# Kernel optimization log

Hardware: AMD Instinct MI355X
Metric: run time of the kernel (lower is better)

## Reference

```python
import jax, jax.numpy as jnp
import numpy as np

# PyTorch LSTM cell with zero initial (h, c): W_hh @ h0 == 0, and c = sigmoid(i)*tanh(g)
# since the forget-gate term f*c0 vanishes. Gate order in torch: i, f, g, o.
# b here is the combined b_ih + b_hh (identical math).

def lstm_step0(x, Wih, b):
    pre = x @ Wih.T + b                      # (N, 4H)
    i, f, g, o = jnp.split(pre, 4, axis=-1)
    c = jax.nn.sigmoid(i) * jnp.tanh(g)
    return jax.nn.sigmoid(o) * jnp.tanh(c)   # (N, H)


def setup_inputs() -> dict:
    key = jax.random.key(0)
    ks = jax.random.split(key, 13)
    num_ts, num_periods, F = 128, 256, 128
    GH, NH, NF = 512, 256, 10
    s = lambda k, shape, fan: (jax.random.normal(k, shape, jnp.float32) / np.sqrt(fan))
    return {
        "X": jax.random.normal(ks[0], (num_ts, num_periods, F), jnp.float32),
        "g_Wih0": s(ks[1], (4 * GH, F), F),
        "g_b0": s(ks[2], (4 * GH,), GH),
        "g_Wih1": s(ks[3], (4 * GH, GH), GH),
        "g_b1": s(ks[4], (4 * GH,), GH),
        "aff_W": s(ks[5], (NF, GH), GH),
        "aff_b": s(ks[6], (NF,), GH),
        "n_Wih0": s(ks[7], (4 * NH, F), F),
        "n_b0": s(ks[8], (4 * NH,), NH),
        "n_Wih1": s(ks[9], (4 * NH, NH), NH),
        "n_b1": s(ks[10], (4 * NH,), NH),
        "noise_W": s(ks[11], (1, NH), NH),
        "noise_b": s(ks[12], (1,), NH),
    }


def reference(X, g_Wih0, g_b0, g_Wih1, g_b1, aff_W, aff_b,
              n_Wih0, n_b0, n_Wih1, n_b1, noise_W, noise_b):
    num_ts, num_periods, num_feats = X.shape
    x = X.reshape(-1, num_feats)             # (num_ts*num_periods, F)

    # Global factor branch: 2-layer LSTM single step from zero state
    hg = lstm_step0(lstm_step0(x, g_Wih0, g_b0), g_Wih1, g_b1)
    hg = jax.nn.relu(hg)
    mus = (hg @ aff_W.T + aff_b).sum(axis=-1).reshape(num_ts, num_periods)

    # Noise branch: 2-layer LSTM single step from zero state
    hn = lstm_step0(lstm_step0(x, n_Wih0, n_b0), n_Wih1, n_b1)
    hn = jax.nn.relu(hn)
    sigmas = jax.nn.softplus(hn @ noise_W.T + noise_b)  # log(1+exp(.)), stable
    sigmas = sigmas.reshape(num_ts, num_periods) + 1e-6
    return mus, sigmas
```

## Files before the change

### kernel.cpp

```cpp
#include <hip/hip_runtime.h>
#include <hip/hip_bf16.h>
#include <hip/hip_fp16.h>

typedef _Float16 h8_t __attribute__((ext_vector_type(8)));
typedef _Float16 h4_t __attribute__((ext_vector_type(4)));
typedef float f4_t __attribute__((ext_vector_type(4)));

#define M_ROWS 32768

__device__ __forceinline__ void gload_lds16(const void* g, void* l) {
  __builtin_amdgcn_global_load_lds((const __attribute__((address_space(1))) void*)g,
                                   (__attribute__((address_space(3))) void*)l, 16, 0, 0);
}

__device__ __forceinline__ float sigmoid_f(float x) { return 1.f / (1.f + __expf(-x)); }
__device__ __forceinline__ float tanh_f(float x) { return 1.f - 2.f / (__expf(2.f * x) + 1.f); }

struct GArgs {
  const _Float16* A;
  const _Float16* W;
  const float* bias;
  _Float16* Hout;
  const float* rvec;
  float* partial;
};

__global__ void prep_all(const float* __restrict__ X, const float* __restrict__ gW0,
                         const float* __restrict__ gW1, const float* __restrict__ nW0,
                         const float* __restrict__ nW1, const float* __restrict__ aff_W,
                         const float* __restrict__ aff_b,
                         _Float16* __restrict__ Xh, _Float16* __restrict__ Wg0,
                         _Float16* __restrict__ Wg1, _Float16* __restrict__ Wn0,
                         _Float16* __restrict__ Wn1,
                         float* __restrict__ pg, float* __restrict__ pn,
                         float* __restrict__ wsum) {
  int b = blockIdx.x;
  const float* s; _Float16* d; int base;
  if (b < 4096)      { s = X;   d = Xh;  base = b; }
  else if (b < 4352) { s = gW0; d = Wg0; base = b - 4096; }
  else if (b < 5376) { s = gW1; d = Wg1; base = b - 4352; }
  else if (b < 5504) { s = nW0; d = Wn0; base = b - 5376; }
  else if (b < 5760) { s = nW1; d = Wn1; base = b - 5504; }
  else if (b < 5888) {
    int i = (b - 5760) * 256 + threadIdx.x;
    pg[i] = 0.f; pn[i] = 0.f;
    return;
  } else {
    int j = (b - 5888) * 256 + threadIdx.x;
    float sum = 0.f;
#pragma unroll
    for (int r = 0; r < 10; ++r) sum += aff_W[r * 512 + j];
    wsum[j] = sum;
    if (j == 0) {
      float bs = 0.f;
#pragma unroll
      for (int r = 0; r < 10; ++r) bs += aff_b[r];
      wsum[512] = bs;
    }
    return;
  }
  int i4 = (base * 256 + threadIdx.x) * 4;
  float4 v = *(const float4*)(s + i4);
  h4_t o;
  o[0] = (_Float16)v.x; o[1] = (_Float16)v.y; o[2] = (_Float16)v.z; o[3] = (_Float16)v.w;
  *(h4_t*)(d + i4) = o;
}

template <int K_DIM, int H_DIM, bool FUSE, int NMT>
__device__ __forceinline__ void gemm_body(const GArgs& ga, int h0, int m_base,
                                          _Float16* As, _Float16* Bs) {
  const int tid = threadIdx.x;
  const int wid = tid >> 6;
  const int lane = tid & 63;
  const int wave_m = wid >> 1;
  const int wave_h = wid & 1;
  const int q = lane >> 4;
  const int tcol = lane & 15;

  constexpr int NT = K_DIM / 64;
  constexpr int TOT = NMT * NT;
  constexpr bool BREUSE = (NMT > 1) && (NT == 2);
  constexpr int A_BYTES = 128 * 64 * 2;
  constexpr int B_BYTES = 3 * 64 * 64 * 2;
  constexpr int A_ELEMS = 128 * 64;
  constexpr int B_ELEMS = 3 * 64 * 64;

  const _Float16* aptr[2]; int aoff[2];
#pragma unroll
  for (int c = 0; c < 2; ++c) {
    int o = ((wid * 2 + c) << 10) + (lane << 4);
    int row = o >> 7, pch = (o >> 4) & 7;
    int lch = pch ^ (row & 7);
    aptr[c] = ga.A + (size_t)(m_base + row) * K_DIM + lch * 8;
    aoff[c] = o;
  }
  const _Float16* bptr[3]; int boff[3];
#pragma unroll
  for (int c = 0; c < 3; ++c) {
    int o = ((wid * 3 + c) << 10) + (lane << 4);
    int pan = o >> 13;
    int row = (o >> 7) & 63, pch = (o >> 4) & 7;
    int lch = pch ^ (row & 7);
    int gbase = (pan == 0 ? 0 : (pan == 1 ? 2 * H_DIM : 3 * H_DIM)) + h0 + row;
    bptr[c] = ga.W + (size_t)gbase * K_DIM + lch * 8;
    boff[c] = o;
  }
  int a_rd[2][2];
#pragma unroll
  for (int ks = 0; ks < 2; ++ks)
#pragma unroll
    for (int mi = 0; mi < 2; ++mi) {
      int r = wave_m * 32 + mi * 16 + tcol;
      int c = ks * 4 + q;
      a_rd[ks][mi] = r * 64 + (c ^ (r & 7)) * 8;
    }
  int b_rd[2][2];
#pragma unroll
  for (int ks = 0; ks < 2; ++ks)
#pragma unroll
    for (int ni = 0; ni < 2; ++ni) {
      int j = wave_h * 32 + ni * 16 + tcol;
      int c = ks * 4 + q;
      b_rd[ks][ni] = j * 64 + (c ^ (j & 7)) * 8;
    }

  const int jcol0 = h0 + wave_h * 32;
  float ebi[2], ebg[2], ebo[2], erv[2];
  if constexpr (NMT > 1) {
#pragma unroll
    for (int ni = 0; ni < 2; ++ni) {
      int j = jcol0 + ni * 16 + tcol;
      ebi[ni] = ga.bias[j];
      ebg[ni] = ga.bias[2 * H_DIM + j];
      ebo[ni] = ga.bias[3 * H_DIM + j];
      if constexpr (FUSE) erv[ni] = ga.rvec[j];
    }
  }

  f4_t acc[3][2][2];
#pragma unroll
  for (int p = 0; p < 3; ++p)
#pragma unroll
    for (int mi = 0; mi < 2; ++mi)
#pragma unroll
      for (int ni = 0; ni < 2; ++ni) acc[p][mi][ni] = (f4_t){0.f, 0.f, 0.f, 0.f};

#pragma unroll
  for (int c = 0; c < 2; ++c) gload_lds16(aptr[c], (char*)As + aoff[c]);
#pragma unroll
  for (int c = 0; c < 3; ++c) gload_lds16(bptr[c], (char*)Bs + boff[c]);
#pragma unroll
  for (int c = 0; c < 2; ++c) aptr[c] += 64;
#pragma unroll
  for (int c = 0; c < 3; ++c) bptr[c] += 64;

#pragma unroll
  for (int s = 0; s < TOT; ++s) {
    const int cur = s & 1;
    const int nxt = cur ^ 1;
    if (s < TOT - 1) {
      const bool stB = (!BREUSE) || (s + 1 < NT);
#pragma unroll
      for (int c = 0; c < 2; ++c) gload_lds16(aptr[c], (char*)As + nxt * A_BYTES + aoff[c]);
      if (stB) {
#pragma unroll
        for (int c = 0; c < 3; ++c) gload_lds16(bptr[c], (char*)Bs + nxt * B_BYTES + boff[c]);
      }
      if (((s + 2) % NT) == 0) {
#pragma unroll
        for (int c = 0; c < 2; ++c) aptr[c] += 128 * K_DIM - (NT - 1) * 64;
      } else {
#pragma unroll
        for (int c = 0; c < 2; ++c) aptr[c] += 64;
      }
      if (stB) {
        if (((s + 2) % NT) == 0) {
#pragma unroll
          for (int c = 0; c < 3; ++c) bptr[c] -= (NT - 1) * 64;
        } else {
#pragma unroll
          for (int c = 0; c < 3; ++c) bptr[c] += 64;
        }
      }
      if (stB) asm volatile("s_waitcnt vmcnt(5)" ::: "memory");
      else     asm volatile("s_waitcnt vmcnt(2)" ::: "memory");
    } else {
      asm volatile("s_waitcnt vmcnt(0)" ::: "memory");
    }
    __builtin_amdgcn_s_barrier();
    asm volatile("" ::: "memory");

#pragma unroll
    for (int ks = 0; ks < 2; ++ks) {
      h8_t af[2];
#pragma unroll
      for (int mi = 0; mi < 2; ++mi) af[mi] = *(const h8_t*)&As[cur * A_ELEMS + a_rd[ks][mi]];
#pragma unroll
      for (int p = 0; p < 3; ++p) {
#pragma unroll
        for (int ni = 0; ni < 2; ++ni) {
          h8_t bf = *(const h8_t*)&Bs[cur * B_ELEMS + p * 4096 + b_rd[ks][ni]];
#pragma unroll
          for (int mi = 0; mi < 2; ++mi)
            acc[p][mi][ni] = __builtin_amdgcn_mfma_f32_16x16x32_f16(af[mi], bf, acc[p][mi][ni], 0, 0, 0);
        }
      }
    }
    asm volatile("" ::: "memory");

    if ((s % NT) == NT - 1) {
      const int mm = s / NT;
      const int mrow0 = m_base + mm * 128 + wave_m * 32;
      if constexpr (!FUSE) {
#pragma unroll
        for (int ni = 0; ni < 2; ++ni) {
          int j = jcol0 + ni * 16 + tcol;
          float bi, bg, bo;
          if constexpr (NMT > 1) { bi = ebi[ni]; bg = ebg[ni]; bo = ebo[ni]; }
          else { bi = ga.bias[j]; bg = ga.bias[2 * H_DIM + j]; bo = ga.bias[3 * H_DIM + j]; }
#pragma unroll
          for (int mi = 0; mi < 2; ++mi)
#pragma unroll
            for (int r = 0; r < 4; ++r) {
              float pi = acc[0][mi][ni][r] + bi;
              float pgt = acc[1][mi][ni][r] + bg;
              float po = acc[2][mi][ni][r] + bo;
              float cc = sigmoid_f(pi) * tanh_f(pgt);
              float hh = sigmoid_f(po) * tanh_f(cc);
              int m = mrow0 + mi * 16 + q * 4 + r;
              ga.Hout[(size_t)m * H_DIM + j] = (_Float16)hh;
            }
        }
      } else {
        float rsum[2][4];
#pragma unroll
        for (int mi = 0; mi < 2; ++mi)
#pragma unroll
          for (int r = 0; r < 4; ++r) rsum[mi][r] = 0.f;
#pragma unroll
        for (int ni = 0; ni < 2; ++ni) {
          int j = jcol0 + ni * 16 + tcol;
          float bi, bg, bo, rv;
          if constexpr (NMT > 1) { bi = ebi[ni]; bg = ebg[ni]; bo = ebo[ni]; rv = erv[ni]; }
          else { bi = ga.bias[j]; bg = ga.bias[2 * H_DIM + j]; bo = ga.bias[3 * H_DIM + j]; rv = ga.rvec[j]; }
#pragma unroll
          for (int mi = 0; mi < 2; ++mi)
#pragma unroll
            for (int r = 0; r < 4; ++r) {
              float pi = acc[0][mi][ni][r] + bi;
              float pgt = acc[1][mi][ni][r] + bg;
              float po = acc[2][mi][ni][r] + bo;
              float cc = sigmoid_f(pi) * tanh_f(pgt);
              float hh = sigmoid_f(po) * tanh_f(cc);
              hh = fmaxf(hh, 0.f);
              rsum[mi][r] += hh * rv;
            }
        }
#pragma unroll
        for (int mi = 0; mi < 2; ++mi)
#pragma unroll
          for (int r = 0; r < 4; ++r) {
            float v = rsum[mi][r];
            v += __shfl_xor(v, 1);
            v += __shfl_xor(v, 2);
            v += __shfl_xor(v, 4);
            v += __shfl_xor(v, 8);
            if (tcol == 0) atomicAdd(&ga.partial[mrow0 + mi * 16 + q * 4 + r], v);
          }
      }
      if (s < TOT - 1) {
#pragma unroll
        for (int p = 0; p < 3; ++p)
#pragma unroll
          for (int mi = 0; mi < 2; ++mi)
#pragma unroll
            for (int ni = 0; ni < 2; ++ni) acc[p][mi][ni] = (f4_t){0.f, 0.f, 0.f, 0.f};
      }
    }

    if (s < TOT - 1) __builtin_amdgcn_s_barrier();
  }
}

__device__ __forceinline__ void swizzle_xy(int& x, int& y) {
  int lin = blockIdx.y * gridDim.x + blockIdx.x;
  int c = lin & 7;
  int r = lin >> 3;
  int xpx = gridDim.x >> 3;
  y = r % 12;
  x = c * xpx + r / 12;
}

__global__ __launch_bounds__(512, 4) void layer1_fused(GArgs g, GArgs n) {
  __shared__ __align__(16) _Float16 As[2 * 128 * 64];
  __shared__ __align__(16) _Float16 Bs[2 * 3 * 64 * 64];
  int x, y; swizzle_xy(x, y);
  if (y < 8) gemm_body<128, 512, false, 2>(g, y * 64, x * 256, As, Bs);
  else       gemm_body<128, 256, false, 2>(n, (y - 8) * 64, x * 256, As, Bs);
}

__global__ __launch_bounds__(512, 4) void layer2_fused(GArgs g, GArgs n) {
  __shared__ __align__(16) _Float16 As[2 * 128 * 64];
  __shared__ __align__(16) _Float16 Bs[2 * 3 * 64 * 64];
  int x, y; swizzle_xy(x, y);
  if (y < 8) gemm_body<512, 512, true, 1>(g, y * 64, x * 128, As, Bs);
  else       gemm_body<256, 256, true, 1>(n, (y - 8) * 64, x * 128, As, Bs);
}

__global__ void finalize(const float* __restrict__ pg, const float* __restrict__ pn,
                         const float* __restrict__ wsum, const float* __restrict__ noise_b,
                         float* __restrict__ out) {
  int i = blockIdx.x * blockDim.x + threadIdx.x;
  out[i] = pg[i] + wsum[512];
  float x = pn[i] + noise_b[0];
  float sp = fmaxf(x, 0.f) + log1pf(expf(-fabsf(x)));
  out[M_ROWS + i] = sp + 1e-6f;
}

extern "C" void kernel_launch(void* const* d_in, const int* in_sizes, int n_in,
                              void* d_out, int out_size, void* d_ws, size_t ws_size,
                              hipStream_t stream) {
  const float* X       = (const float*)d_in[0];
  const float* g_Wih0  = (const float*)d_in[1];
  const float* g_b0    = (const float*)d_in[2];
  const float* g_Wih1  = (const float*)d_in[3];
  const float* g_b1    = (const float*)d_in[4];
  const float* aff_W   = (const float*)d_in[5];
  const float* aff_b   = (const float*)d_in[6];
  const float* n_Wih0  = (const float*)d_in[7];
  const float* n_b0    = (const float*)d_in[8];
  const float* n_Wih1  = (const float*)d_in[9];
  const float* n_b1    = (const float*)d_in[10];
  const float* noise_W = (const float*)d_in[11];
  const float* noise_b = (const float*)d_in[12];
  float* out = (float*)d_out;

  char* w = (char*)d_ws;
  _Float16* Xh  = (_Float16*)w; w += (size_t)M_ROWS * 128 * 2;
  _Float16* Wg0 = (_Float16*)w; w += 2048 * 128 * 2;
  _Float16* Wg1 = (_Float16*)w; w += 2048 * 512 * 2;
  _Float16* Wn0 = (_Float16*)w; w += 1024 * 128 * 2;
  _Float16* Wn1 = (_Float16*)w; w += 1024 * 256 * 2;
  _Float16* h1g = (_Float16*)w; w += (size_t)M_ROWS * 512 * 2;
  _Float16* h1n = (_Float16*)w; w += (size_t)M_ROWS * 256 * 2;
  float* pg   = (float*)w; w += (size_t)M_ROWS * 4;
  float* pn   = (float*)w; w += (size_t)M_ROWS * 4;
  float* wsum = (float*)w; w += 4096;

  prep_all<<<5890, 256, 0, stream>>>(X, g_Wih0, g_Wih1, n_Wih0, n_Wih1, aff_W, aff_b,
                                     Xh, Wg0, Wg1, Wn0, Wn1, pg, pn, wsum);

  GArgs l1g = {Xh, Wg0, g_b0, h1g, nullptr, nullptr};
  GArgs l1n = {Xh, Wn0, n_b0, h1n, nullptr, nullptr};
  layer1_fused<<<dim3(128, 12), 512, 0, stream>>>(l1g, l1n);

  GArgs l2g = {h1g, Wg1, g_b1, nullptr, wsum, pg};
  GArgs l2n = {h1n, Wn1, n_b1, nullptr, noise_W, pn};
  layer2_fused<<<dim3(256, 12), 512, 0, stream>>>(l2g, l2n);

  finalize<<<M_ROWS / 256, 256, 0, stream>>>(pg, pn, wsum, noise_b, out);
}
```

Before: 266.0 us.

## Restructure layer-1 GEMM to keep A tile resident and sweep weight panels

Replaces the layer-1 kernel with a panel kernel that loads a 128-row block of X (full K=128) into LDS once. Each block then iterates over six 64-column weight panels that span both the global and noise branches, double-buffering only the weight tiles. The goal is to cut redundant reloads of the X rows and reduce grid launch granularity. It also removes the register-cached bias values in favour of per-epilogue loads, and generalises the block swizzle to use gridDim.y. In exchange, each block runs a longer serial loop with less block-level parallelism (512 blocks).

```diff
diff --git a/kernel.cpp b/kernel.cpp
--- a/kernel.cpp
+++ b/kernel.cpp
@@ -125,17 +125,6 @@
     }
 
   const int jcol0 = h0 + wave_h * 32;
-  float ebi[2], ebg[2], ebo[2], erv[2];
-  if constexpr (NMT > 1) {
-#pragma unroll
-    for (int ni = 0; ni < 2; ++ni) {
-      int j = jcol0 + ni * 16 + tcol;
-      ebi[ni] = ga.bias[j];
-      ebg[ni] = ga.bias[2 * H_DIM + j];
-      ebo[ni] = ga.bias[3 * H_DIM + j];
-      if constexpr (FUSE) erv[ni] = ga.rvec[j];
-    }
-  }
 
   f4_t acc[3][2][2];
 #pragma unroll
@@ -215,9 +204,9 @@
 #pragma unroll
         for (int ni = 0; ni < 2; ++ni) {
           int j = jcol0 + ni * 16 + tcol;
-          float bi, bg, bo;
-          if constexpr (NMT > 1) { bi = ebi[ni]; bg = ebg[ni]; bo = ebo[ni]; }
-          else { bi = ga.bias[j]; bg = ga.bias[2 * H_DIM + j]; bo = ga.bias[3 * H_DIM + j]; }
+          float bi = ga.bias[j];
+          float bg = ga.bias[2 * H_DIM + j];
+          float bo = ga.bias[3 * H_DIM + j];
 #pragma unroll
           for (int mi = 0; mi < 2; ++mi)
 #pragma unroll
@@ -240,9 +229,10 @@
 #pragma unroll
         for (int ni = 0; ni < 2; ++ni) {
           int j = jcol0 + ni * 16 + tcol;
-          float bi, bg, bo, rv;
-          if constexpr (NMT > 1) { bi = ebi[ni]; bg = ebg[ni]; bo = ebo[ni]; rv = erv[ni]; }
-          else { bi = ga.bias[j]; bg = ga.bias[2 * H_DIM + j]; bo = ga.bias[3 * H_DIM + j]; rv = ga.rvec[j]; }
+          float bi = ga.bias[j];
+          float bg = ga.bias[2 * H_DIM + j];
+          float bo = ga.bias[3 * H_DIM + j];
+          float rv = ga.rvec[j];
 #pragma unroll
           for (int mi = 0; mi < 2; ++mi)
 #pragma unroll
@@ -287,16 +277,163 @@
   int c = lin & 7;
   int r = lin >> 3;
   int xpx = gridDim.x >> 3;
-  y = r % 12;
-  x = c * xpx + r / 12;
-}
-
-__global__ __launch_bounds__(512, 4) void layer1_fused(GArgs g, GArgs n) {
+  y = r % gridDim.y;
+  x = c * xpx + r / gridDim.y;
+}
+
+__global__ __launch_bounds__(512, 4) void layer1_panel(GArgs g, GArgs n) {
   __shared__ __align__(16) _Float16 As[2 * 128 * 64];
   __shared__ __align__(16) _Float16 Bs[2 * 3 * 64 * 64];
-  int x, y; swizzle_xy(x, y);
-  if (y < 8) gemm_body<128, 512, false, 2>(g, y * 64, x * 256, As, Bs);
-  else       gemm_body<128, 256, false, 2>(n, (y - 8) * 64, x * 256, As, Bs);
+  int x, yh; swizzle_xy(x, yh);
+  const int tid = threadIdx.x;
+  const int wid = tid >> 6;
+  const int lane = tid & 63;
+  const int wave_m = wid >> 1;
+  const int wave_h = wid & 1;
+  const int q = lane >> 4;
+  const int tcol = lane & 15;
+  const int m0 = x * 128;
+
+  int b_pan[3], b_row[3], b_lch[3], b_off[3];
+#pragma unroll
+  for (int c = 0; c < 3; ++c) {
+    int o = ((wid * 3 + c) << 10) + (lane << 4);
+    b_pan[c] = o >> 13;
+    b_row[c] = (o >> 7) & 63;
+    int pch = (o >> 4) & 7;
+    b_lch[c] = pch ^ (b_row[c] & 7);
+    b_off[c] = o;
+  }
+  int a_rd[2][2];
+#pragma unroll
+  for (int ks = 0; ks < 2; ++ks)
+#pragma unroll
+    for (int mi = 0; mi < 2; ++mi) {
+      int r = wave_m * 32 + mi * 16 + tcol;
+      int c = ks * 4 + q;
+      a_rd[ks][mi] = r * 64 + (c ^ (r & 7)) * 8;
+    }
+  int b_rd[2][2];
+#pragma unroll
+  for (int ks = 0; ks < 2; ++ks)
+#pragma unroll
+    for (int ni = 0; ni < 2; ++ni) {
+      int j = wave_h * 32 + ni * 16 + tcol;
+      int c = ks * 4 + q;
+      b_rd[ks][ni] = j * 64 + (c ^ (j & 7)) * 8;
+    }
+
+  f4_t acc[3][2][2];
+#pragma unroll
+  for (int p = 0; p < 3; ++p)
+#pragma unroll
+    for (int mi = 0; mi < 2; ++mi)
+#pragma unroll
+      for (int ni = 0; ni < 2; ++ni) acc[p][mi][ni] = (f4_t){0.f, 0.f, 0.f, 0.f};
+
+#pragma unroll
+  for (int kt = 0; kt < 2; ++kt)
+#pragma unroll
+    for (int c = 0; c < 2; ++c) {
+      int o = ((wid * 2 + c) << 10) + (lane << 4);
+      int row = o >> 7, pch = (o >> 4) & 7;
+      int lch = pch ^ (row & 7);
+      gload_lds16(g.A + (size_t)(m0 + row) * 128 + kt * 64 + lch * 8,
+                  (char*)As + kt * 16384 + o);
+    }
+  {
+    const int pnl = yh * 6;
+    const _Float16* W = pnl < 8 ? g.W : n.W;
+    const int H = pnl < 8 ? 512 : 256;
+    const int h0 = pnl < 8 ? pnl * 64 : (pnl - 8) * 64;
+#pragma unroll
+    for (int c = 0; c < 3; ++c) {
+      int gb = b_pan[c] == 0 ? 0 : (b_pan[c] == 1 ? 2 * H : 3 * H);
+      gload_lds16(W + (size_t)(gb + h0 + b_row[c]) * 128 + b_lch[c] * 8,
+                  (char*)Bs + b_off[c]);
+    }
+  }
+
+#pragma unroll
+  for (int s = 0; s < 12; ++s) {
+    const int kt = s & 1;
+    const int cur = s & 1;
+    const int pnl = yh * 6 + (s >> 1);
+    if (s < 11) {
+      const int s1 = s + 1;
+      const int pnl1 = yh * 6 + (s1 >> 1);
+      const int kt1 = s1 & 1;
+      const int nxt = cur ^ 1;
+      const _Float16* W = pnl1 < 8 ? g.W : n.W;
+      const int H = pnl1 < 8 ? 512 : 256;
+      const int h0 = pnl1 < 8 ? pnl1 * 64 : (pnl1 - 8) * 64;
+#pragma unroll
+      for (int c = 0; c < 3; ++c) {
+        int gb = b_pan[c] == 0 ? 0 : (b_pan[c] == 1 ? 2 * H : 3 * H);
+        gload_lds16(W + (size_t)(gb + h0 + b_row[c]) * 128 + kt1 * 64 + b_lch[c] * 8,
+                    (char*)Bs + nxt * 24576 + b_off[c]);
+      }
+      asm volatile("s_waitcnt vmcnt(3)" ::: "memory");
+    } else {
+      asm volatile("s_waitcnt vmcnt(0)" ::: "memory");
+    }
+    __builtin_amdgcn_s_barrier();
+    asm volatile("" ::: "memory");
+
+#pragma unroll
+    for (int ks = 0; ks < 2; ++ks) {
+      h8_t af[2];
+#pragma unroll
+      for (int mi = 0; mi < 2; ++mi) af[mi] = *(const h8_t*)&As[kt * 8192 + a_rd[ks][mi]];
+#pragma unroll
+      for (int p = 0; p < 3; ++p) {
+#pragma unroll
+        for (int ni = 0; ni < 2; ++ni) {
+          h8_t bf = *(const h8_t*)&Bs[cur * 12288 + p * 4096 + b_rd[ks][ni]];
+#pragma unroll
+          for (int mi = 0; mi < 2; ++mi)
+            acc[p][mi][ni] = __builtin_amdgcn_mfma_f32_16x16x32_f16(af[mi], bf, acc[p][mi][ni], 0, 0, 0);
+        }
+      }
+    }
+    asm volatile("" ::: "memory");
+
+    if (kt == 1) {
+      const GArgs& ga = pnl < 8 ? g : n;
+      const int H = pnl < 8 ? 512 : 256;
+      const int h0 = pnl < 8 ? pnl * 64 : (pnl - 8) * 64;
+      const int mrow0 = m0 + wave_m * 32;
+#pragma unroll
+      for (int ni = 0; ni < 2; ++ni) {
+        int j = h0 + wave_h * 32 + ni * 16 + tcol;
+        float bi = ga.bias[j];
+        float bg = ga.bias[2 * H + j];
+        float bo = ga.bias[3 * H + j];
+#pragma unroll
+        for (int mi = 0; mi < 2; ++mi)
+#pragma unroll
+          for (int r = 0; r < 4; ++r) {
+            float pi = acc[0][mi][ni][r] + bi;
+            float pgt = acc[1][mi][ni][r] + bg;
+            float po = acc[2][mi][ni][r] + bo;
+            float cc = sigmoid_f(pi) * tanh_f(pgt);
+            float hh = sigmoid_f(po) * tanh_f(cc);
+            int m = mrow0 + mi * 16 + q * 4 + r;
+            ga.Hout[(size_t)m * H + j] = (_Float16)hh;
+          }
+      }
+      if (s < 11) {
+#pragma unroll
+        for (int p = 0; p < 3; ++p)
+#pragma unroll
+          for (int mi = 0; mi < 2; ++mi)
+#pragma unroll
+            for (int ni = 0; ni < 2; ++ni) acc[p][mi][ni] = (f4_t){0.f, 0.f, 0.f, 0.f};
+      }
+    }
+
+    if (s < 11) __builtin_amdgcn_s_barrier();
+  }
 }
 
 __global__ __launch_bounds__(512, 4) void layer2_fused(GArgs g, GArgs n) {
@@ -352,7 +489,7 @@
 
   GArgs l1g = {Xh, Wg0, g_b0, h1g, nullptr, nullptr};
   GArgs l1n = {Xh, Wn0, n_b0, h1n, nullptr, nullptr};
-  layer1_fused<<<dim3(128, 12), 512, 0, stream>>>(l1g, l1n);
+  layer1_panel<<<dim3(256, 2), 512, 0, stream>>>(l1g, l1n);
 
   GArgs l2g = {h1g, Wg1, g_b1, nullptr, wsum, pg};
   GArgs l2n = {h1n, Wn1, n_b1, nullptr, noise_W, pn};
```

Result: slower. 281.9 us (+6.0%).
